# Optimization experiments

Measured on AMD Instinct MI355X. Metric: run time of the kernel, lower is better.

## Reference

```python
import jax, jax.numpy as jnp
import numpy as np


def setup_inputs() -> dict:
    key = jax.random.key(0)
    k1, k2, k3, k4 = jax.random.split(key, 4)
    I, Q, P, S, N = 512000, 128, 1, 8, 4000
    x = jax.random.normal(k1, (I, Q), dtype=jnp.float32)
    beta_u = jax.random.normal(k2, (Q, P, S), dtype=jnp.float32)
    beta_z = jax.random.normal(k3, (Q, P, S), dtype=jnp.float32)
    i = jnp.sort(jax.random.randint(k4, (I,), 0, N, dtype=jnp.int64))
    return {"x": x, "beta_u": beta_u, "beta_z": beta_z, "i": i, "n_bags": N}


def _scatter_softmax(u, seg, num_segments):
    # numerically stable softmax over variable-size segments (bags)
    seg_max = jax.ops.segment_max(u, seg, num_segments=num_segments)  # [N,P,S]
    e = jnp.exp(u - seg_max[seg])                                     # [I,P,S]
    denom = jax.ops.segment_sum(e, seg, num_segments=num_segments)    # [N,P,S]
    return e / denom[seg]


def reference(x, beta_u, beta_z, i, n_bags):
    # b = rms of beta_z over latent dim -> [1,P,S]; eta = normalized beta_z
    b = jnp.sqrt(jnp.mean(beta_z ** 2, axis=0, keepdims=True))
    eta = beta_z / b
    # gather -> per-instance projections -> scatter softmax -> segment pooling
    u = jnp.einsum('iq,qps->ips', x, beta_u)      # [I,P,S]
    w = _scatter_softmax(u, i, n_bags)            # [I,P,S]
    z = jnp.einsum('iq,qps->ips', x, eta)         # [I,P,S]
    xmil = jax.ops.segment_sum(w * z, i, num_segments=n_bags)  # [N,P,S]
    # normalize across bags (torch .std is unbiased, ddof=1), rescale by b
    mean = jnp.mean(xmil, axis=0)
    std = jnp.std(xmil, axis=0, ddof=1)
    return b * (xmil - mean) / std
```

## Files before the change

### kernel.cpp

```cpp
#include <hip/hip_runtime.h>
#include <hip/hip_bf16.h>


#define QDIM 128
#define C8 8

typedef __attribute__((ext_vector_type(8))) short s8v;
typedef __attribute__((ext_vector_type(4))) float f4v;

__device__ __forceinline__ void split8(const float xs[8], s8v& AH, s8v& AL) {
#pragma unroll
    for (int j = 0; j < 8; ++j) {
        const float xv = xs[j];
        const __hip_bfloat16 hb = __float2bfloat16(xv);
        const float hf = __bfloat162float(hb);
        const __hip_bfloat16 lb = __float2bfloat16(xv - hf);
        unsigned short hr, lr;
        __builtin_memcpy(&hr, &hb, 2);
        __builtin_memcpy(&lr, &lb, 2);
        AH[j] = (short)hr;
        AL[j] = (short)lr;
    }
}

__global__ void mixmil_bounds(const int* __restrict__ seg, int I, int N,
                              int* __restrict__ bs)
{
    int k = blockIdx.x * blockDim.x + threadIdx.x;
    if (k > I) return;
    int a    = (k < I) ? seg[k]     : N;
    int prev = (k > 0) ? seg[k - 1] : -1;
    for (int j = prev + 1; j <= a; ++j) bs[j] = k;
}

__global__ __launch_bounds__(256) void mixmil_fused(
    const float* __restrict__ x,
    const float* __restrict__ bu,
    const float* __restrict__ bz,
    const int*   __restrict__ bs,
    int I, int N,
    float* __restrict__ xmil)
{
    __shared__ float XT[4 * 2 * 2048];

    const int t    = threadIdx.x;
    const int lane = t & 63;
    const int wv   = t >> 6;

    const int mybag = blockIdx.x * 4 + wv;
    if (mybag >= N) return;
    const int lo = bs[mybag];
    const int hi = bs[mybag + 1];

    const int bn  = lane & 15;
    const int bkg = lane >> 4;
    s8v BH[4], BL[4];
    const float* wcol = (bn < 8) ? (bu + bn) : (bz + (bn - 8));
#pragma unroll
    for (int kc = 0; kc < 4; ++kc) {
        float ws[8];
#pragma unroll
        for (int j = 0; j < 8; ++j)
            ws[j] = wcol[(size_t)(kc * 32 + bkg * 8 + j) * 8];
        split8(ws, BH[kc], BL[kc]);
    }

    float* const myXT = &XT[wv * 4096];
    const int rl   = lane >> 5;
    const int c4l  = lane & 31;

    const int nt = (hi - lo + 15) >> 4;

#define STAGE(J, SEL)                                                          \
    {                                                                          \
        const int base_ = lo + (J) * 16;                                       \
        _Pragma("unroll")                                                      \
        for (int i = 0; i < 8; ++i) {                                          \
            const int r_ = i * 2 + rl;                                         \
            int grow_ = base_ + r_;                                            \
            if (grow_ >= hi) grow_ = hi - 1;                                   \
            const int c4g_ = c4l ^ (r_ & 7);                                   \
            const float* src_ = x + (size_t)grow_ * QDIM + 4 * (size_t)c4g_;   \
            __builtin_amdgcn_global_load_lds(                                  \
                (const __attribute__((address_space(1))) unsigned int*)src_,   \
                (__attribute__((address_space(3))) unsigned int*)              \
                    &myXT[(SEL) * 2048 + i * 256],                             \
                16, 0, 0);                                                     \
        }                                                                      \
    }

    float lsum = 0.f, asum = 0.f;

    const int am  = lane & 15;
    const int akg = lane >> 4;
    const int sw  = am & 7;

    if (nt > 0) STAGE(0, 0);

    for (int j = 0; j < nt; ++j) {
        const int sel = j & 1;
        if (j + 1 < nt) {
            STAGE(j + 1, sel ^ 1);
            asm volatile("s_waitcnt vmcnt(8)" ::: "memory");
        } else {
            asm volatile("s_waitcnt vmcnt(0)" ::: "memory");
        }
        __builtin_amdgcn_sched_barrier(0);

        const float* buf = &myXT[sel * 2048];

        f4v acc = {0.f, 0.f, 0.f, 0.f};
#pragma unroll
        for (int kc = 0; kc < 4; ++kc) {
            const int c4a = kc * 8 + akg * 2;
            const float4 xa = *(const float4*)&buf[am * QDIM + 4 * ((c4a    ) ^ sw)];
            const float4 xb = *(const float4*)&buf[am * QDIM + 4 * ((c4a + 1) ^ sw)];
            const float xs[8] = {xa.x, xa.y, xa.z, xa.w, xb.x, xb.y, xb.z, xb.w};
            s8v AH, AL;
            split8(xs, AH, AL);
            acc = __builtin_amdgcn_mfma_f32_16x16x32_bf16(AH, BH[kc], acc, 0, 0, 0);
            acc = __builtin_amdgcn_mfma_f32_16x16x32_bf16(AH, BL[kc], acc, 0, 0, 0);
            acc = __builtin_amdgcn_mfma_f32_16x16x32_bf16(AL, BH[kc], acc, 0, 0, 0);
        }

        const int base = lo + j * 16;
        const int r0   = (lane >> 4) * 4;
#pragma unroll
        for (int i = 0; i < 4; ++i) {
            const float uv = acc[i];
            const float zv = __shfl_xor(uv, 8);
            const bool valid = (base + r0 + i) < hi;
            if ((lane & 15) < 8 && valid) {
                const float e = __expf(uv);
                lsum += e;
                asum = fmaf(e, zv, asum);
            }
        }
    }

    lsum += __shfl_xor(lsum, 16);
    asum += __shfl_xor(asum, 16);
    lsum += __shfl_xor(lsum, 32);
    asum += __shfl_xor(asum, 32);

    if (lane < 8)
        xmil[(size_t)mybag * 8 + lane] = (hi > lo) ? (asum / lsum) : 0.f;
#undef STAGE
}

__global__ __launch_bounds__(256) void mixmil_statsout(
    const float* __restrict__ xmil,
    const float* __restrict__ bz,
    int N, int total,
    float* __restrict__ out)
{
    double s[8], qq[8];
    float t2[8];
#pragma unroll
    for (int c = 0; c < 8; ++c) { s[c] = 0.0; qq[c] = 0.0; t2[c] = 0.f; }

    for (int r = threadIdx.x; r < N; r += 256) {
        const float* row = xmil + (size_t)r * 8;
#pragma unroll
        for (int c = 0; c < 8; ++c) {
            float v = row[c];
            s[c] += v;
            qq[c] += (double)v * (double)v;
        }
    }
    for (int r = threadIdx.x; r < QDIM; r += 256) {
        const float* row = bz + (size_t)r * 8;
#pragma unroll
        for (int c = 0; c < 8; ++c) { float v = row[c]; t2[c] = fmaf(v, v, t2[c]); }
    }

    for (int off = 32; off; off >>= 1) {
#pragma unroll
        for (int c = 0; c < 8; ++c) {
            s[c]  += __shfl_xor(s[c], off);
            qq[c] += __shfl_xor(qq[c], off);
            t2[c] += __shfl_xor(t2[c], off);
        }
    }

    __shared__ double S[4][8], QQ[4][8];
    __shared__ float T2[4][8];
    __shared__ float fb[8], fm[8], fr[8];
    const int w = threadIdx.x >> 6;
    if ((threadIdx.x & 63) == 0) {
#pragma unroll
        for (int c = 0; c < 8; ++c) { S[w][c] = s[c]; QQ[w][c] = qq[c]; T2[w][c] = t2[c]; }
    }
    __syncthreads();
    if (threadIdx.x < 8) {
        const int c = threadIdx.x;
        double ss = S[0][c] + S[1][c] + S[2][c] + S[3][c];
        double qs = QQ[0][c] + QQ[1][c] + QQ[2][c] + QQ[3][c];
        float  tt = T2[0][c] + T2[1][c] + T2[2][c] + T2[3][c];
        double mean = ss / (double)N;
        double var  = (qs - ss * ss / (double)N) / (double)(N - 1);
        fb[c] = sqrtf(tt / (float)QDIM);
        fm[c] = (float)mean;
        fr[c] = (float)(1.0 / sqrt(var));
    }
    __syncthreads();

    const int e = blockIdx.x * 256 + threadIdx.x;
    if (e < total) {
        const int c = e & 7;
        out[e] = fb[c] * (xmil[e] - fm[c]) * fr[c];
    }
}

extern "C" void kernel_launch(void* const* d_in, const int* in_sizes, int n_in,
                              void* d_out, int out_size, void* d_ws, size_t ws_size,
                              hipStream_t stream) {
    const float* x  = (const float*)d_in[0];
    const float* bu = (const float*)d_in[1];
    const float* bz = (const float*)d_in[2];
    const int*   sg = (const int*)d_in[3];

    const int I = in_sizes[0] / QDIM;
    const int N = out_size / C8;

    float* xmil = (float*)d_ws;
    int*   bs   = (int*)(xmil + (size_t)N * C8);

    mixmil_bounds<<<(I + 256) / 256, 256, 0, stream>>>(sg, I, N, bs);

    mixmil_fused<<<(N + 3) / 4, 256, 0, stream>>>(x, bu, bz, bs, I, N, xmil);

    const int total = N * C8;
    mixmil_statsout<<<(total + 255) / 256, 256, 0, stream>>>(
        xmil, bz, N, total, (float*)d_out);
}
```

Measured before the change: 63.35 us.

## Process two bags per wavefront with a continuous cross-bag prefetch pipeline

Each wavefront now handles two bags (b0 and b0+bstride), so the grid is halved. Both bags' 16-row chunks run through one double-buffered global-to-LDS pipeline, so the second bag's first chunk is prefetched while the first bag finishes. This amortises the per-wave B-fragment setup and the pipeline fill and drain across two bags. In exchange there are fewer waves to hide latency and extra per-chunk branching to pick the base row and row limit.

```diff
diff --git a/kernel.cpp b/kernel.cpp
--- a/kernel.cpp
+++ b/kernel.cpp
@@ -38,7 +38,7 @@
     const float* __restrict__ bu,
     const float* __restrict__ bz,
     const int*   __restrict__ bs,
-    int I, int N,
+    int I, int N, int bstride,
     float* __restrict__ xmil)
 {
     __shared__ float XT[4 * 2 * 2048];
@@ -47,10 +47,22 @@
     const int lane = t & 63;
     const int wv   = t >> 6;
 
-    const int mybag = blockIdx.x * 4 + wv;
-    if (mybag >= N) return;
-    const int lo = bs[mybag];
-    const int hi = bs[mybag + 1];
+    const int b0 = blockIdx.x * 4 + wv;
+    const int b1 = b0 + bstride;
+    if (b0 >= N) return;
+
+    const int lo0 = bs[b0], hi0 = bs[b0 + 1];
+    int lo1 = 0, hi1 = 0;
+    if (b1 < N) { lo1 = bs[b1]; hi1 = bs[b1 + 1]; }
+    const int nt0 = (hi0 - lo0 + 15) >> 4;
+    const int nt1 = (hi1 - lo1 + 15) >> 4;
+    const int total = nt0 + nt1;
+
+    if (lane < 8) {
+        if (nt0 == 0) xmil[(size_t)b0 * 8 + lane] = 0.f;
+        if (b1 < N && nt1 == 0) xmil[(size_t)b1 * 8 + lane] = 0.f;
+    }
+    if (total == 0) return;
 
     const int bn  = lane & 15;
     const int bkg = lane >> 4;
@@ -66,25 +78,28 @@
     }
 
     float* const myXT = &XT[wv * 4096];
-    const int rl   = lane >> 5;
-    const int c4l  = lane & 31;
-
-    const int nt = (hi - lo + 15) >> 4;
-
-#define STAGE(J, SEL)                                                          \
+    const int rl  = lane >> 5;
+    const int c4l = lane & 31;
+
+#define CH_BASE(C) (((C) >= nt0) ? (lo1 + (((C) - nt0) << 4)) : (lo0 + ((C) << 4)))
+#define CH_LIM(C)  (((C) >= nt0) ? hi1 : hi0)
+
+#define STAGE(C)                                                               \
     {                                                                          \
-        const int base_ = lo + (J) * 16;                                       \
+        const int base_ = CH_BASE(C);                                          \
+        const int lim_  = CH_LIM(C);                                           \
+        float* dst_ = &myXT[((C) & 1) * 2048];                                 \
         _Pragma("unroll")                                                      \
         for (int i = 0; i < 8; ++i) {                                          \
             const int r_ = i * 2 + rl;                                         \
             int grow_ = base_ + r_;                                            \
-            if (grow_ >= hi) grow_ = hi - 1;                                   \
+            if (grow_ >= lim_) grow_ = lim_ - 1;                               \
             const int c4g_ = c4l ^ (r_ & 7);                                   \
             const float* src_ = x + (size_t)grow_ * QDIM + 4 * (size_t)c4g_;   \
             __builtin_amdgcn_global_load_lds(                                  \
                 (const __attribute__((address_space(1))) unsigned int*)src_,   \
                 (__attribute__((address_space(3))) unsigned int*)              \
-                    &myXT[(SEL) * 2048 + i * 256],                             \
+                    (dst_ + i * 256),                                          \
                 16, 0, 0);                                                     \
         }                                                                      \
     }
@@ -95,19 +110,18 @@
     const int akg = lane >> 4;
     const int sw  = am & 7;
 
-    if (nt > 0) STAGE(0, 0);
-
-    for (int j = 0; j < nt; ++j) {
-        const int sel = j & 1;
-        if (j + 1 < nt) {
-            STAGE(j + 1, sel ^ 1);
+    STAGE(0);
+
+    for (int c = 0; c < total; ++c) {
+        if (c + 1 < total) {
+            STAGE(c + 1);
             asm volatile("s_waitcnt vmcnt(8)" ::: "memory");
         } else {
             asm volatile("s_waitcnt vmcnt(0)" ::: "memory");
         }
         __builtin_amdgcn_sched_barrier(0);
 
-        const float* buf = &myXT[sel * 2048];
+        const float* buf = &myXT[(c & 1) * 2048];
 
         f4v acc = {0.f, 0.f, 0.f, 0.f};
 #pragma unroll
@@ -123,29 +137,38 @@
             acc = __builtin_amdgcn_mfma_f32_16x16x32_bf16(AL, BH[kc], acc, 0, 0, 0);
         }
 
-        const int base = lo + j * 16;
+        const int base = CH_BASE(c);
+        const int lim  = CH_LIM(c);
         const int r0   = (lane >> 4) * 4;
 #pragma unroll
         for (int i = 0; i < 4; ++i) {
             const float uv = acc[i];
             const float zv = __shfl_xor(uv, 8);
-            const bool valid = (base + r0 + i) < hi;
+            const bool valid = (base + r0 + i) < lim;
             if ((lane & 15) < 8 && valid) {
                 const float e = __expf(uv);
                 lsum += e;
                 asum = fmaf(e, zv, asum);
             }
         }
-    }
-
-    lsum += __shfl_xor(lsum, 16);
-    asum += __shfl_xor(asum, 16);
-    lsum += __shfl_xor(lsum, 32);
-    asum += __shfl_xor(asum, 32);
-
-    if (lane < 8)
-        xmil[(size_t)mybag * 8 + lane] = (hi > lo) ? (asum / lsum) : 0.f;
+
+        const bool fin0 = (c == nt0 - 1);
+        const bool fin1 = (c == total - 1) && (nt1 > 0);
+        if (fin0 || fin1) {
+            float ls = lsum, as = asum;
+            ls += __shfl_xor(ls, 16);
+            as += __shfl_xor(as, 16);
+            ls += __shfl_xor(ls, 32);
+            as += __shfl_xor(as, 32);
+            const int bag = fin0 ? b0 : b1;
+            if (lane < 8)
+                xmil[(size_t)bag * 8 + lane] = as / ls;
+            lsum = 0.f; asum = 0.f;
+        }
+    }
 #undef STAGE
+#undef CH_BASE
+#undef CH_LIM
 }
 
 __global__ __launch_bounds__(256) void mixmil_statsout(
@@ -223,12 +246,15 @@
     const int I = in_sizes[0] / QDIM;
     const int N = out_size / C8;
 
+    const int nblk = (N + 7) / 8;
+    const int bstride = nblk * 4;
+
     float* xmil = (float*)d_ws;
     int*   bs   = (int*)(xmil + (size_t)N * C8);
 
     mixmil_bounds<<<(I + 256) / 256, 256, 0, stream>>>(sg, I, N, bs);
 
-    mixmil_fused<<<(N + 3) / 4, 256, 0, stream>>>(x, bu, bz, bs, I, N, xmil);
+    mixmil_fused<<<nblk, 256, 0, stream>>>(x, bu, bz, bs, I, N, bstride, xmil);
 
     const int total = N * C8;
     mixmil_statsout<<<(total + 255) / 256, 256, 0, stream>>>(
```

Measured after the change: 62.62 us. About the same (-1.1%).
